# Kernel tuning notes

Measured on AMD Instinct MI355X. Metric: run time of the kernel, lower is better.

## Reference

```python
import jax, jax.numpy as jnp
import numpy as np

N_NODES = 50000
N_EDGES = 800000
F_IN = 32
H = 128
LN_EPS = 1e-5


def _gcn_layer(h, src, tgt, w_self, b_self, w_neigh, b_neigh):
    # h: [N, D]; src/tgt: [E]
    n = h.shape[0]
    self_feat = h @ w_self + b_self                      # [N, Dout]
    src_feat = h[src]                                    # [E, D] gather
    agg = jax.ops.segment_sum(src_feat, tgt, num_segments=n)          # [N, D]
    cnt = jax.ops.segment_sum(jnp.ones((src.shape[0],), h.dtype), tgt,
                              num_segments=n)[:, None]   # [N, 1]
    agg = agg / jnp.maximum(cnt, 1.0)
    return self_feat + agg @ w_neigh + b_neigh


def _layer_norm(x, gamma, beta):
    mu = jnp.mean(x, axis=-1, keepdims=True)
    var = jnp.mean(jnp.square(x - mu), axis=-1, keepdims=True)
    return (x - mu) * jax.lax.rsqrt(var + LN_EPS) * gamma + beta


def setup_inputs() -> dict:
    key = jax.random.key(0)
    ks = jax.random.split(key, 16)
    s_in = 1.0 / np.sqrt(F_IN)
    s_h = 1.0 / np.sqrt(H)
    inp = {
        "x": jax.random.normal(ks[0], (N_NODES, F_IN), jnp.float32),
        "edge_index": jax.random.randint(ks[1], (2, N_EDGES), 0, N_NODES, jnp.int64)
        if jax.config.jax_enable_x64 else
        jax.random.randint(ks[1], (2, N_EDGES), 0, N_NODES, jnp.int32),
        "w_in": jax.random.uniform(ks[2], (F_IN, H), jnp.float32, -s_in, s_in),
        "b_in": jax.random.uniform(ks[3], (H,), jnp.float32, -s_in, s_in),
        "ws0": jax.random.uniform(ks[4], (H, H), jnp.float32, -s_h, s_h),
        "bs0": jax.random.uniform(ks[5], (H,), jnp.float32, -s_h, s_h),
        "wn0": jax.random.uniform(ks[6], (H, H), jnp.float32, -s_h, s_h),
        "bn0": jax.random.uniform(ks[7], (H,), jnp.float32, -s_h, s_h),
        "g0": jnp.ones((H,), jnp.float32),
        "be0": jnp.zeros((H,), jnp.float32),
        "ws1": jax.random.uniform(ks[8], (H, H), jnp.float32, -s_h, s_h),
        "bs1": jax.random.uniform(ks[9], (H,), jnp.float32, -s_h, s_h),
        "wn1": jax.random.uniform(ks[10], (H, H), jnp.float32, -s_h, s_h),
        "bn1": jax.random.uniform(ks[11], (H,), jnp.float32, -s_h, s_h),
        "g1": jnp.ones((H,), jnp.float32),
        "be1": jnp.zeros((H,), jnp.float32),
    }
    return inp


def reference(x, edge_index, w_in, b_in, ws0, bs0, wn0, bn0, g0, be0,
              ws1, bs1, wn1, bn1, g1, be1):
    src, tgt = edge_index[0], edge_index[1]
    h = jax.nn.relu(x @ w_in + b_in)                     # input_proj + relu
    # layer 0 (intermediate): gcn -> LN -> relu -> dropout(eval=id) -> residual
    residual = h
    h = _gcn_layer(h, src, tgt, ws0, bs0, wn0, bn0)
    h = _layer_norm(h, g0, be0)
    h = jax.nn.relu(h) + residual
    # layer 1 (final): gcn -> LN
    h = _gcn_layer(h, src, tgt, ws1, bs1, wn1, bn1)
    h = _layer_norm(h, g1, be1)
    return h
```

## Files before the change

kernel.cpp:

```cpp
#include <hip/hip_runtime.h>

#define H 128
#define CAP 64
typedef unsigned short ushort_t;
typedef __bf16 bf16x8 __attribute__((ext_vector_type(8)));
typedef float f32x4 __attribute__((ext_vector_type(4)));
typedef float f32x2 __attribute__((ext_vector_type(2)));

__device__ __forceinline__ float bf2f(ushort_t b) {
    return __uint_as_float(((unsigned int)b) << 16);
}
__device__ __forceinline__ ushort_t f2bf(float f) {
    unsigned int u = __float_as_uint(f);
    unsigned int r = (u + 0x7fffu + ((u >> 16) & 1u)) >> 16;
    return (ushort_t)r;
}
__device__ __forceinline__ unsigned char f2fp8(float f) {
    int r = __builtin_amdgcn_cvt_pk_fp8_f32(f, f, 0, false);
    return (unsigned char)(r & 0xff);
}

__device__ __forceinline__
void pack_one(int idx, const float* __restrict__ W0, const float* __restrict__ W1,
              const float* __restrict__ b0, const float* __restrict__ b1,
              ushort_t* __restrict__ Wpack, float* __restrict__ bsum,
              int Ksplit, int K)
{
    int total = K * 16;
    if (idx < total) {
        int l = idx & 63, tt = (idx >> 6) & 7, s = idx >> 9;
        int c = tt * 16 + (l & 15);
        int kb = s * 32 + ((l >> 4) & 3) * 8;
#pragma unroll
        for (int j = 0; j < 8; ++j) {
            int k = kb + j;
            float v = (k < Ksplit) ? W0[(size_t)k * H + c]
                                   : W1[(size_t)(k - Ksplit) * H + c];
            Wpack[(size_t)idx * 8 + j] = f2bf(v);
        }
    }
    if (idx < H) bsum[idx] = b0[idx] + (b1 ? b1[idx] : 0.f);
}

__global__ __launch_bounds__(256)
void k_prep(const float* __restrict__ x, ushort_t* __restrict__ xb, int n4,
            const float* __restrict__ w_in, const float* __restrict__ b_in,
            const float* __restrict__ ws0, const float* __restrict__ bs0,
            const float* __restrict__ wn0, const float* __restrict__ bn0,
            const float* __restrict__ ws1, const float* __restrict__ bs1,
            const float* __restrict__ wn1, const float* __restrict__ bn1,
            ushort_t* __restrict__ Wpin, float* __restrict__ bin,
            ushort_t* __restrict__ Wp0, float* __restrict__ bsm0,
            ushort_t* __restrict__ Wp1, float* __restrict__ bsm1,
            int* __restrict__ fl, int N, int gN)
{
    int b = blockIdx.x, t = threadIdx.x;
    if (b < 2) {
        pack_one(b * 256 + t, w_in, w_in, b_in, nullptr, Wpin, bin, 32, 32);
    } else if (b < 18) {
        pack_one((b - 2) * 256 + t, ws0, wn0, bs0, bn0, Wp0, bsm0, 128, 256);
    } else if (b < 34) {
        pack_one((b - 18) * 256 + t, ws1, wn1, bs1, bn1, Wp1, bsm1, 128, 256);
    } else if (b < 34 + gN) {
        int i = (b - 34) * 256 + t;
        if (i < N) fl[i] = 0;
    } else {
        int i = (b - 34 - gN) * 256 + t;
        if (i < n4) {
            float4 v = ((const float4*)x)[i];
            ushort_t* o = xb + (size_t)i * 4;
            o[0] = f2bf(v.x); o[1] = f2bf(v.y); o[2] = f2bf(v.z); o[3] = f2bf(v.w);
        }
    }
}

template<int K, int DO_LN, int RESREL, int RELU, int OUTBF, int HQ>
__global__ __launch_bounds__(256)
void k_gemm_ln(const ushort_t* __restrict__ A, int lda,
               const ushort_t* __restrict__ Wpack,
               const float* __restrict__ bias,
               const float* __restrict__ g, const float* __restrict__ be,
               const ushort_t* __restrict__ resid, int ldr,
               float* __restrict__ Cf, ushort_t* __restrict__ Cb,
               unsigned char* __restrict__ hq,
               int ldc, int M)
{
    constexpr int NS = K / 32;
    __shared__ ushort_t Bs[NS * 8 * 64 * 8];
    const int t = threadIdx.x;
    {
        const uint4* wsrc = (const uint4*)Wpack;
        uint4* wdst = (uint4*)Bs;
        constexpr int CH = K * 16;
#pragma unroll
        for (int i = t; i < CH; i += 256) wdst[i] = wsrc[i];
    }
    __syncthreads();

    const int wave = t >> 6, lane = t & 63;
    const int quad = lane >> 4, l16 = lane & 15;
    const int m0 = blockIdx.x * 128 + wave * 32;

    f32x4 acc[2][8];
#pragma unroll
    for (int mt = 0; mt < 2; ++mt)
#pragma unroll
        for (int nt = 0; nt < 8; ++nt) acc[mt][nt] = (f32x4){0.f, 0.f, 0.f, 0.f};

    bf16x8 afrag[NS][2];
#pragma unroll
    for (int s = 0; s < NS; ++s)
#pragma unroll
        for (int mt = 0; mt < 2; ++mt) {
            int row = m0 + mt * 16 + l16;
            if (row >= M) row = M - 1;
            afrag[s][mt] = *(const bf16x8*)(A + (size_t)row * lda + s * 32 + quad * 8);
        }

    const bf16x8* bfr = (const bf16x8*)Bs;
#pragma unroll
    for (int s = 0; s < NS; ++s)
#pragma unroll
        for (int nt = 0; nt < 8; ++nt) {
            bf16x8 b = bfr[(s * 8 + nt) * 64 + lane];
#pragma unroll
            for (int mt = 0; mt < 2; ++mt)
                acc[mt][nt] = __builtin_amdgcn_mfma_f32_16x16x32_bf16(
                    afrag[s][mt], b, acc[mt][nt], 0, 0, 0);
        }

    float bv[8], gv[8], bev[8];
#pragma unroll
    for (int nt = 0; nt < 8; ++nt) {
        int c = nt * 16 + l16;
        bv[nt] = bias[c];
        if (DO_LN) { gv[nt] = g[c]; bev[nt] = be[c]; }
    }

#pragma unroll
    for (int mt = 0; mt < 2; ++mt)
#pragma unroll
        for (int r = 0; r < 4; ++r) {
            int row = m0 + mt * 16 + quad * 4 + r;
            float v[8];
#pragma unroll
            for (int nt = 0; nt < 8; ++nt) v[nt] = acc[mt][nt][r] + bv[nt];
            if (DO_LN) {
                float s1 = 0.f, s2 = 0.f;
#pragma unroll
                for (int nt = 0; nt < 8; ++nt) { s1 += v[nt]; s2 += v[nt] * v[nt]; }
#pragma unroll
                for (int mk = 1; mk < 16; mk <<= 1) {
                    s1 += __shfl_xor(s1, mk);
                    s2 += __shfl_xor(s2, mk);
                }
                float mu = s1 * (1.f / H);
                float var = s2 * (1.f / H) - mu * mu;
                float rs = rsqrtf(var + 1e-5f);
#pragma unroll
                for (int nt = 0; nt < 8; ++nt)
                    v[nt] = (v[nt] - mu) * rs * gv[nt] + bev[nt];
            }
            if (row < M) {
#pragma unroll
                for (int nt = 0; nt < 8; ++nt) {
                    int c = nt * 16 + l16;
                    float y = v[nt];
                    if (RELU) y = fmaxf(y, 0.f);
                    if (RESREL)
                        y = fmaxf(y, 0.f) + bf2f(resid[(size_t)row * ldr + c]);
                    if (OUTBF) Cb[(size_t)row * ldc + c] = f2bf(y);
                    else       Cf[(size_t)row * ldc + c] = y;
                    if (HQ) hq[(size_t)row * H + c] = f2fp8(y);
                }
            }
        }
}

__global__ __launch_bounds__(256)
void k_agg(const unsigned char* __restrict__ hq, const int* __restrict__ fl,
           const ushort_t* __restrict__ col, ushort_t* __restrict__ out, int n)
{
    int node = blockIdx.x * 4 + (threadIdx.x >> 6);
    if (node >= n) return;
    int lane = threadIdx.x & 63;
    int grp = lane >> 4, li = lane & 15;
    int cnt = fl[node];
    int m = cnt < CAP ? cnt : CAP;
    int beg = node * CAP, end = beg + m;
    float s[8];
#pragma unroll
    for (int j = 0; j < 8; ++j) s[j] = 0.f;

    int e = beg;
    for (; e + 16 <= end; e += 16) {
        uint2 v[4];
#pragma unroll
        for (int q = 0; q < 4; ++q) {
            int r = col[e + 4 * q + grp];
            v[q] = *(const uint2*)(hq + (size_t)r * 128 + li * 8);
        }
#pragma unroll
        for (int q = 0; q < 4; ++q) {
            f32x2 a0 = __builtin_amdgcn_cvt_pk_f32_fp8(v[q].x, false);
            f32x2 a1 = __builtin_amdgcn_cvt_pk_f32_fp8(v[q].x, true);
            f32x2 a2 = __builtin_amdgcn_cvt_pk_f32_fp8(v[q].y, false);
            f32x2 a3 = __builtin_amdgcn_cvt_pk_f32_fp8(v[q].y, true);
            s[0] += a0.x; s[1] += a0.y; s[2] += a1.x; s[3] += a1.y;
            s[4] += a2.x; s[5] += a2.y; s[6] += a3.x; s[7] += a3.y;
        }
    }
    if (e + 8 <= end) {
        uint2 v[2];
#pragma unroll
        for (int q = 0; q < 2; ++q) {
            int r = col[e + 4 * q + grp];
            v[q] = *(const uint2*)(hq + (size_t)r * 128 + li * 8);
        }
#pragma unroll
        for (int q = 0; q < 2; ++q) {
            f32x2 a0 = __builtin_amdgcn_cvt_pk_f32_fp8(v[q].x, false);
            f32x2 a1 = __builtin_amdgcn_cvt_pk_f32_fp8(v[q].x, true);
            f32x2 a2 = __builtin_amdgcn_cvt_pk_f32_fp8(v[q].y, false);
            f32x2 a3 = __builtin_amdgcn_cvt_pk_f32_fp8(v[q].y, true);
            s[0] += a0.x; s[1] += a0.y; s[2] += a1.x; s[3] += a1.y;
            s[4] += a2.x; s[5] += a2.y; s[6] += a3.x; s[7] += a3.y;
        }
        e += 8;
    }
    if (e + 4 <= end) {
        int r = col[e + grp];
        uint2 v0 = *(const uint2*)(hq + (size_t)r * 128 + li * 8);
        f32x2 a0 = __builtin_amdgcn_cvt_pk_f32_fp8(v0.x, false);
        f32x2 a1 = __builtin_amdgcn_cvt_pk_f32_fp8(v0.x, true);
        f32x2 a2 = __builtin_amdgcn_cvt_pk_f32_fp8(v0.y, false);
        f32x2 a3 = __builtin_amdgcn_cvt_pk_f32_fp8(v0.y, true);
        s[0] += a0.x; s[1] += a0.y; s[2] += a1.x; s[3] += a1.y;
        s[4] += a2.x; s[5] += a2.y; s[6] += a3.x; s[7] += a3.y;
        e += 4;
    }
    for (; e < end; ++e) {
        if (grp == 0) {
            int r = col[e];
            uint2 v0 = *(const uint2*)(hq + (size_t)r * 128 + li * 8);
            f32x2 a0 = __builtin_amdgcn_cvt_pk_f32_fp8(v0.x, false);
            f32x2 a1 = __builtin_amdgcn_cvt_pk_f32_fp8(v0.x, true);
            f32x2 a2 = __builtin_amdgcn_cvt_pk_f32_fp8(v0.y, false);
            f32x2 a3 = __builtin_amdgcn_cvt_pk_f32_fp8(v0.y, true);
            s[0] += a0.x; s[1] += a0.y; s[2] += a1.x; s[3] += a1.y;
            s[4] += a2.x; s[5] += a2.y; s[6] += a3.x; s[7] += a3.y;
        }
    }
#pragma unroll
    for (int j = 0; j < 8; ++j) {
        s[j] += __shfl_xor(s[j], 16);
        s[j] += __shfl_xor(s[j], 32);
    }
    if (grp == 0) {
        float inv = 1.f / fmaxf((float)cnt, 1.f);
        uint4 o;
        o.x = ((unsigned)f2bf(s[1] * inv) << 16) | f2bf(s[0] * inv);
        o.y = ((unsigned)f2bf(s[3] * inv) << 16) | f2bf(s[2] * inv);
        o.z = ((unsigned)f2bf(s[5] * inv) << 16) | f2bf(s[4] * inv);
        o.w = ((unsigned)f2bf(s[7] * inv) << 16) | f2bf(s[6] * inv);
        *(uint4*)(out + (size_t)node * 256 + li * 8) = o;
    }
}

#define FILL_CHUNK 4096
__global__ __launch_bounds__(256)
void k_fill(const int* __restrict__ srcs, const int* __restrict__ tgts,
            int* __restrict__ fl, ushort_t* __restrict__ col, int E)
{
    int range = blockIdx.x & 7;
    int chunk = blockIdx.x >> 3;
    int lim = chunk * FILL_CHUNK + FILL_CHUNK;
    if (lim > E) lim = E;
    for (int i = chunk * FILL_CHUNK + threadIdx.x; i < lim; i += 256) {
        int t = tgts[i];
        if ((t >> 13) == range) {
            int p = atomicAdd(&fl[t], 1);
            if (p < CAP) col[t * CAP + p] = (ushort_t)srcs[i];
        }
    }
}

extern "C" void kernel_launch(void* const* d_in, const int* in_sizes, int n_in,
                              void* d_out, int out_size, void* d_ws, size_t ws_size,
                              hipStream_t stream)
{
    const float* x    = (const float*)d_in[0];
    const int*   ei   = (const int*)d_in[1];
    const float* w_in = (const float*)d_in[2];
    const float* b_in = (const float*)d_in[3];
    const float* ws0  = (const float*)d_in[4];
    const float* bs0  = (const float*)d_in[5];
    const float* wn0  = (const float*)d_in[6];
    const float* bn0  = (const float*)d_in[7];
    const float* g0   = (const float*)d_in[8];
    const float* be0  = (const float*)d_in[9];
    const float* ws1  = (const float*)d_in[10];
    const float* bs1  = (const float*)d_in[11];
    const float* wn1  = (const float*)d_in[12];
    const float* bn1  = (const float*)d_in[13];
    const float* g1   = (const float*)d_in[14];
    const float* be1  = (const float*)d_in[15];

    const int N = in_sizes[0] / 32;
    const int E = in_sizes[1] / 2;
    const int* srcs = ei;
    const int* tgts = ei + E;

    char* w = (char*)d_ws;
    ushort_t* Acat0 = (ushort_t*)w;  w += (size_t)N * 256 * 2;
    ushort_t* Acat1 = (ushort_t*)w;  w += (size_t)N * 256 * 2;
    unsigned char* hq0 = (unsigned char*)w;  w += (size_t)N * H;
    unsigned char* hq1 = (unsigned char*)w;  w += (size_t)N * H;
    ushort_t* x_bf  = (ushort_t*)w;  w += (size_t)N * 32 * 2;
    ushort_t* Wpin  = (ushort_t*)w;  w += 32 * H * 2;
    ushort_t* Wp0   = (ushort_t*)w;  w += 256 * H * 2;
    ushort_t* Wp1   = (ushort_t*)w;  w += 256 * H * 2;
    float* bin  = (float*)w;         w += H * 4;
    float* bsm0 = (float*)w;         w += H * 4;
    float* bsm1 = (float*)w;         w += H * 4;
    int* fl     = (int*)w;           w += (size_t)N * 4;
    ushort_t* col = (ushort_t*)w;    w += (size_t)N * CAP * 2;

    int n4 = N * 32 / 4;
    int gN = (N + 255) / 256;
    int gC = (n4 + 255) / 256;
    int gM = (N + 127) / 128;
    int gF = 8 * ((E + FILL_CHUNK - 1) / FILL_CHUNK);

    k_prep<<<34 + gN + gC, 256, 0, stream>>>(
        x, x_bf, n4, w_in, b_in, ws0, bs0, wn0, bn0, ws1, bs1, wn1, bn1,
        Wpin, bin, Wp0, bsm0, Wp1, bsm1, fl, N, gN);

    k_fill<<<gF, 256, 0, stream>>>(srcs, tgts, fl, col, E);

    k_gemm_ln<32, 0, 0, 1, 1, 1><<<gM, 256, 0, stream>>>(
        x_bf, 32, Wpin, bin, nullptr, nullptr, nullptr, 0,
        nullptr, Acat0, hq0, 256, N);

    k_agg<<<(N + 3) / 4, 256, 0, stream>>>(hq0, fl, col, Acat0 + 128, N);
    k_gemm_ln<256, 1, 1, 0, 1, 1><<<gM, 256, 0, stream>>>(
        Acat0, 256, Wp0, bsm0, g0, be0, Acat0, 256,
        nullptr, Acat1, hq1, 256, N);

    k_agg<<<(N + 3) / 4, 256, 0, stream>>>(hq1, fl, col, Acat1 + 128, N);
    k_gemm_ln<256, 1, 0, 0, 0, 0><<<gM, 256, 0, stream>>>(
        Acat1, 256, Wp1, bsm1, g1, be1, nullptr, 0,
        (float*)d_out, nullptr, nullptr, H, N);
}
```

Baseline: 227.9 us.

## Fuse neighbor aggregation into per-layer GEMM+LayerNorm kernel

Merges the separate gather-mean aggregation kernel and the GEMM+LN kernel into one per-layer kernel. Each wave aggregates its 16 nodes into shared memory and then feeds them straight into the MFMA as the second half of K. This removes the bf16 agg round trip through global memory and two launches. In exchange each wave serialises over 16 nodes of gather work, uses 64-row blocks, and stages the weights into LDS in two halves with extra barriers, which may reduce latency hiding for the gathers.

```diff
diff --git a/kernel.cpp b/kernel.cpp
--- a/kernel.cpp
+++ b/kernel.cpp
@@ -2,6 +2,7 @@
 
 #define H 128
 #define CAP 64
+#define FILL_CHUNK 4096
 typedef unsigned short ushort_t;
 typedef __bf16 bf16x8 __attribute__((ext_vector_type(8)));
 typedef float f32x4 __attribute__((ext_vector_type(4)));
@@ -74,200 +75,6 @@
     }
 }
 
-template<int K, int DO_LN, int RESREL, int RELU, int OUTBF, int HQ>
-__global__ __launch_bounds__(256)
-void k_gemm_ln(const ushort_t* __restrict__ A, int lda,
-               const ushort_t* __restrict__ Wpack,
-               const float* __restrict__ bias,
-               const float* __restrict__ g, const float* __restrict__ be,
-               const ushort_t* __restrict__ resid, int ldr,
-               float* __restrict__ Cf, ushort_t* __restrict__ Cb,
-               unsigned char* __restrict__ hq,
-               int ldc, int M)
-{
-    constexpr int NS = K / 32;
-    __shared__ ushort_t Bs[NS * 8 * 64 * 8];
-    const int t = threadIdx.x;
-    {
-        const uint4* wsrc = (const uint4*)Wpack;
-        uint4* wdst = (uint4*)Bs;
-        constexpr int CH = K * 16;
-#pragma unroll
-        for (int i = t; i < CH; i += 256) wdst[i] = wsrc[i];
-    }
-    __syncthreads();
-
-    const int wave = t >> 6, lane = t & 63;
-    const int quad = lane >> 4, l16 = lane & 15;
-    const int m0 = blockIdx.x * 128 + wave * 32;
-
-    f32x4 acc[2][8];
-#pragma unroll
-    for (int mt = 0; mt < 2; ++mt)
-#pragma unroll
-        for (int nt = 0; nt < 8; ++nt) acc[mt][nt] = (f32x4){0.f, 0.f, 0.f, 0.f};
-
-    bf16x8 afrag[NS][2];
-#pragma unroll
-    for (int s = 0; s < NS; ++s)
-#pragma unroll
-        for (int mt = 0; mt < 2; ++mt) {
-            int row = m0 + mt * 16 + l16;
-            if (row >= M) row = M - 1;
-            afrag[s][mt] = *(const bf16x8*)(A + (size_t)row * lda + s * 32 + quad * 8);
-        }
-
-    const bf16x8* bfr = (const bf16x8*)Bs;
-#pragma unroll
-    for (int s = 0; s < NS; ++s)
-#pragma unroll
-        for (int nt = 0; nt < 8; ++nt) {
-            bf16x8 b = bfr[(s * 8 + nt) * 64 + lane];
-#pragma unroll
-            for (int mt = 0; mt < 2; ++mt)
-                acc[mt][nt] = __builtin_amdgcn_mfma_f32_16x16x32_bf16(
-                    afrag[s][mt], b, acc[mt][nt], 0, 0, 0);
-        }
-
-    float bv[8], gv[8], bev[8];
-#pragma unroll
-    for (int nt = 0; nt < 8; ++nt) {
-        int c = nt * 16 + l16;
-        bv[nt] = bias[c];
-        if (DO_LN) { gv[nt] = g[c]; bev[nt] = be[c]; }
-    }
-
-#pragma unroll
-    for (int mt = 0; mt < 2; ++mt)
-#pragma unroll
-        for (int r = 0; r < 4; ++r) {
-            int row = m0 + mt * 16 + quad * 4 + r;
-            float v[8];
-#pragma unroll
-            for (int nt = 0; nt < 8; ++nt) v[nt] = acc[mt][nt][r] + bv[nt];
-            if (DO_LN) {
-                float s1 = 0.f, s2 = 0.f;
-#pragma unroll
-                for (int nt = 0; nt < 8; ++nt) { s1 += v[nt]; s2 += v[nt] * v[nt]; }
-#pragma unroll
-                for (int mk = 1; mk < 16; mk <<= 1) {
-                    s1 += __shfl_xor(s1, mk);
-                    s2 += __shfl_xor(s2, mk);
-                }
-                float mu = s1 * (1.f / H);
-                float var = s2 * (1.f / H) - mu * mu;
-                float rs = rsqrtf(var + 1e-5f);
-#pragma unroll
-                for (int nt = 0; nt < 8; ++nt)
-                    v[nt] = (v[nt] - mu) * rs * gv[nt] + bev[nt];
-            }
-            if (row < M) {
-#pragma unroll
-                for (int nt = 0; nt < 8; ++nt) {
-                    int c = nt * 16 + l16;
-                    float y = v[nt];
-                    if (RELU) y = fmaxf(y, 0.f);
-                    if (RESREL)
-                        y = fmaxf(y, 0.f) + bf2f(resid[(size_t)row * ldr + c]);
-                    if (OUTBF) Cb[(size_t)row * ldc + c] = f2bf(y);
-                    else       Cf[(size_t)row * ldc + c] = y;
-                    if (HQ) hq[(size_t)row * H + c] = f2fp8(y);
-                }
-            }
-        }
-}
-
-__global__ __launch_bounds__(256)
-void k_agg(const unsigned char* __restrict__ hq, const int* __restrict__ fl,
-           const ushort_t* __restrict__ col, ushort_t* __restrict__ out, int n)
-{
-    int node = blockIdx.x * 4 + (threadIdx.x >> 6);
-    if (node >= n) return;
-    int lane = threadIdx.x & 63;
-    int grp = lane >> 4, li = lane & 15;
-    int cnt = fl[node];
-    int m = cnt < CAP ? cnt : CAP;
-    int beg = node * CAP, end = beg + m;
-    float s[8];
-#pragma unroll
-    for (int j = 0; j < 8; ++j) s[j] = 0.f;
-
-    int e = beg;
-    for (; e + 16 <= end; e += 16) {
-        uint2 v[4];
-#pragma unroll
-        for (int q = 0; q < 4; ++q) {
-            int r = col[e + 4 * q + grp];
-            v[q] = *(const uint2*)(hq + (size_t)r * 128 + li * 8);
-        }
-#pragma unroll
-        for (int q = 0; q < 4; ++q) {
-            f32x2 a0 = __builtin_amdgcn_cvt_pk_f32_fp8(v[q].x, false);
-            f32x2 a1 = __builtin_amdgcn_cvt_pk_f32_fp8(v[q].x, true);
-            f32x2 a2 = __builtin_amdgcn_cvt_pk_f32_fp8(v[q].y, false);
-            f32x2 a3 = __builtin_amdgcn_cvt_pk_f32_fp8(v[q].y, true);
-            s[0] += a0.x; s[1] += a0.y; s[2] += a1.x; s[3] += a1.y;
-            s[4] += a2.x; s[5] += a2.y; s[6] += a3.x; s[7] += a3.y;
-        }
-    }
-    if (e + 8 <= end) {
-        uint2 v[2];
-#pragma unroll
-        for (int q = 0; q < 2; ++q) {
-            int r = col[e + 4 * q + grp];
-            v[q] = *(const uint2*)(hq + (size_t)r * 128 + li * 8);
-        }
-#pragma unroll
-        for (int q = 0; q < 2; ++q) {
-            f32x2 a0 = __builtin_amdgcn_cvt_pk_f32_fp8(v[q].x, false);
-            f32x2 a1 = __builtin_amdgcn_cvt_pk_f32_fp8(v[q].x, true);
-            f32x2 a2 = __builtin_amdgcn_cvt_pk_f32_fp8(v[q].y, false);
-            f32x2 a3 = __builtin_amdgcn_cvt_pk_f32_fp8(v[q].y, true);
-            s[0] += a0.x; s[1] += a0.y; s[2] += a1.x; s[3] += a1.y;
-            s[4] += a2.x; s[5] += a2.y; s[6] += a3.x; s[7] += a3.y;
-        }
-        e += 8;
-    }
-    if (e + 4 <= end) {
-        int r = col[e + grp];
-        uint2 v0 = *(const uint2*)(hq + (size_t)r * 128 + li * 8);
-        f32x2 a0 = __builtin_amdgcn_cvt_pk_f32_fp8(v0.x, false);
-        f32x2 a1 = __builtin_amdgcn_cvt_pk_f32_fp8(v0.x, true);
-        f32x2 a2 = __builtin_amdgcn_cvt_pk_f32_fp8(v0.y, false);
-        f32x2 a3 = __builtin_amdgcn_cvt_pk_f32_fp8(v0.y, true);
-        s[0] += a0.x; s[1] += a0.y; s[2] += a1.x; s[3] += a1.y;
-        s[4] += a2.x; s[5] += a2.y; s[6] += a3.x; s[7] += a3.y;
-        e += 4;
-    }
-    for (; e < end; ++e) {
-        if (grp == 0) {
-            int r = col[e];
-            uint2 v0 = *(const uint2*)(hq + (size_t)r * 128 + li * 8);
-            f32x2 a0 = __builtin_amdgcn_cvt_pk_f32_fp8(v0.x, false);
-            f32x2 a1 = __builtin_amdgcn_cvt_pk_f32_fp8(v0.x, true);
-            f32x2 a2 = __builtin_amdgcn_cvt_pk_f32_fp8(v0.y, false);
-            f32x2 a3 = __builtin_amdgcn_cvt_pk_f32_fp8(v0.y, true);
-            s[0] += a0.x; s[1] += a0.y; s[2] += a1.x; s[3] += a1.y;
-            s[4] += a2.x; s[5] += a2.y; s[6] += a3.x; s[7] += a3.y;
-        }
-    }
-#pragma unroll
-    for (int j = 0; j < 8; ++j) {
-        s[j] += __shfl_xor(s[j], 16);
-        s[j] += __shfl_xor(s[j], 32);
-    }
-    if (grp == 0) {
-        float inv = 1.f / fmaxf((float)cnt, 1.f);
-        uint4 o;
-        o.x = ((unsigned)f2bf(s[1] * inv) << 16) | f2bf(s[0] * inv);
-        o.y = ((unsigned)f2bf(s[3] * inv) << 16) | f2bf(s[2] * inv);
-        o.z = ((unsigned)f2bf(s[5] * inv) << 16) | f2bf(s[4] * inv);
-        o.w = ((unsigned)f2bf(s[7] * inv) << 16) | f2bf(s[6] * inv);
-        *(uint4*)(out + (size_t)node * 256 + li * 8) = o;
-    }
-}
-
-#define FILL_CHUNK 4096
 __global__ __launch_bounds__(256)
 void k_fill(const int* __restrict__ srcs, const int* __restrict__ tgts,
             int* __restrict__ fl, ushort_t* __restrict__ col, int E)
@@ -281,6 +88,253 @@
         if ((t >> 13) == range) {
             int p = atomicAdd(&fl[t], 1);
             if (p < CAP) col[t * CAP + p] = (ushort_t)srcs[i];
+        }
+    }
+}
+
+__global__ __launch_bounds__(256)
+void k_gin(const ushort_t* __restrict__ A,
+           const ushort_t* __restrict__ Wpack, const float* __restrict__ bias,
+           ushort_t* __restrict__ hout, unsigned char* __restrict__ hqout, int M)
+{
+    __shared__ ushort_t Bs[512 * 8];
+    const int t = threadIdx.x;
+    {
+        const uint4* wsrc = (const uint4*)Wpack;
+        uint4* wdst = (uint4*)Bs;
+#pragma unroll
+        for (int i = t; i < 512; i += 256) wdst[i] = wsrc[i];
+    }
+    __syncthreads();
+
+    const int wave = t >> 6, lane = t & 63;
+    const int quad = lane >> 4, l16 = lane & 15;
+    const int m0 = blockIdx.x * 128 + wave * 32;
+    const bf16x8* bfr = (const bf16x8*)Bs;
+
+    f32x4 acc[2][8];
+#pragma unroll
+    for (int mt = 0; mt < 2; ++mt)
+#pragma unroll
+        for (int nt = 0; nt < 8; ++nt) acc[mt][nt] = (f32x4){0.f, 0.f, 0.f, 0.f};
+
+    bf16x8 afrag[2];
+#pragma unroll
+    for (int mt = 0; mt < 2; ++mt) {
+        int row = m0 + mt * 16 + l16;
+        if (row >= M) row = M - 1;
+        afrag[mt] = *(const bf16x8*)(A + (size_t)row * 32 + quad * 8);
+    }
+#pragma unroll
+    for (int nt = 0; nt < 8; ++nt) {
+        bf16x8 b = bfr[nt * 64 + lane];
+#pragma unroll
+        for (int mt = 0; mt < 2; ++mt)
+            acc[mt][nt] = __builtin_amdgcn_mfma_f32_16x16x32_bf16(
+                afrag[mt], b, acc[mt][nt], 0, 0, 0);
+    }
+
+    float bv[8];
+#pragma unroll
+    for (int nt = 0; nt < 8; ++nt) bv[nt] = bias[nt * 16 + l16];
+
+#pragma unroll
+    for (int mt = 0; mt < 2; ++mt)
+#pragma unroll
+        for (int r = 0; r < 4; ++r) {
+            int row = m0 + mt * 16 + quad * 4 + r;
+            if (row < M) {
+#pragma unroll
+                for (int nt = 0; nt < 8; ++nt) {
+                    int c = nt * 16 + l16;
+                    float y = fmaxf(acc[mt][nt][r] + bv[nt], 0.f);
+                    hout[(size_t)row * H + c] = f2bf(y);
+                    hqout[(size_t)row * H + c] = f2fp8(y);
+                }
+            }
+        }
+}
+
+template<int L0>
+__global__ __launch_bounds__(256)
+void k_layer(const ushort_t* __restrict__ h, const unsigned char* __restrict__ hq,
+             const int* __restrict__ fl, const ushort_t* __restrict__ col,
+             const ushort_t* __restrict__ Wpack, const float* __restrict__ bias,
+             const float* __restrict__ g, const float* __restrict__ be,
+             ushort_t* __restrict__ hout, unsigned char* __restrict__ hqout,
+             float* __restrict__ fout, int M)
+{
+    __shared__ ushort_t Bs[4 * 512 * 8];
+    __shared__ ushort_t aggBuf[4][16 * 136];
+    const int t = threadIdx.x, wave = t >> 6, lane = t & 63;
+    const int quad = lane >> 4, l16 = lane & 15;
+    const int m0 = blockIdx.x * 64 + wave * 16;
+
+    bf16x8 afrag[8];
+#pragma unroll
+    for (int s = 0; s < 4; ++s) {
+        int row = m0 + l16; if (row >= M) row = M - 1;
+        afrag[s] = *(const bf16x8*)(h + (size_t)row * H + s * 32 + quad * 8);
+    }
+
+    {
+        const uint4* wsrc = (const uint4*)Wpack;
+        uint4* wdst = (uint4*)Bs;
+#pragma unroll
+        for (int i = t; i < 2048; i += 256) wdst[i] = wsrc[i];
+    }
+
+    ushort_t* ab = aggBuf[wave];
+    for (int j = 0; j < 16; ++j) {
+        int node = m0 + j;
+        if (node >= M) break;
+        int cnt = fl[node];
+        int m = cnt < CAP ? cnt : CAP;
+        int beg = node * CAP;
+        float s[8];
+#pragma unroll
+        for (int k = 0; k < 8; ++k) s[k] = 0.f;
+        int e = 0;
+        for (; e + 16 <= m; e += 16) {
+            uint2 v[4];
+#pragma unroll
+            for (int q = 0; q < 4; ++q) {
+                int r = col[beg + e + 4 * q + quad];
+                v[q] = *(const uint2*)(hq + (size_t)r * H + l16 * 8);
+            }
+#pragma unroll
+            for (int q = 0; q < 4; ++q) {
+                f32x2 a0 = __builtin_amdgcn_cvt_pk_f32_fp8(v[q].x, false);
+                f32x2 a1 = __builtin_amdgcn_cvt_pk_f32_fp8(v[q].x, true);
+                f32x2 a2 = __builtin_amdgcn_cvt_pk_f32_fp8(v[q].y, false);
+                f32x2 a3 = __builtin_amdgcn_cvt_pk_f32_fp8(v[q].y, true);
+                s[0] += a0.x; s[1] += a0.y; s[2] += a1.x; s[3] += a1.y;
+                s[4] += a2.x; s[5] += a2.y; s[6] += a3.x; s[7] += a3.y;
+            }
+        }
+        if (e + 8 <= m) {
+            uint2 v[2];
+#pragma unroll
+            for (int q = 0; q < 2; ++q) {
+                int r = col[beg + e + 4 * q + quad];
+                v[q] = *(const uint2*)(hq + (size_t)r * H + l16 * 8);
+            }
+#pragma unroll
+            for (int q = 0; q < 2; ++q) {
+                f32x2 a0 = __builtin_amdgcn_cvt_pk_f32_fp8(v[q].x, false);
+                f32x2 a1 = __builtin_amdgcn_cvt_pk_f32_fp8(v[q].x, true);
+                f32x2 a2 = __builtin_amdgcn_cvt_pk_f32_fp8(v[q].y, false);
+                f32x2 a3 = __builtin_amdgcn_cvt_pk_f32_fp8(v[q].y, true);
+                s[0] += a0.x; s[1] += a0.y; s[2] += a1.x; s[3] += a1.y;
+                s[4] += a2.x; s[5] += a2.y; s[6] += a3.x; s[7] += a3.y;
+            }
+            e += 8;
+        }
+        if (e + 4 <= m) {
+            int r = col[beg + e + quad];
+            uint2 v0 = *(const uint2*)(hq + (size_t)r * H + l16 * 8);
+            f32x2 a0 = __builtin_amdgcn_cvt_pk_f32_fp8(v0.x, false);
+            f32x2 a1 = __builtin_amdgcn_cvt_pk_f32_fp8(v0.x, true);
+            f32x2 a2 = __builtin_amdgcn_cvt_pk_f32_fp8(v0.y, false);
+            f32x2 a3 = __builtin_amdgcn_cvt_pk_f32_fp8(v0.y, true);
+            s[0] += a0.x; s[1] += a0.y; s[2] += a1.x; s[3] += a1.y;
+            s[4] += a2.x; s[5] += a2.y; s[6] += a3.x; s[7] += a3.y;
+            e += 4;
+        }
+        if (quad < m - e) {
+            int r = col[beg + e + quad];
+            uint2 v0 = *(const uint2*)(hq + (size_t)r * H + l16 * 8);
+            f32x2 a0 = __builtin_amdgcn_cvt_pk_f32_fp8(v0.x, false);
+            f32x2 a1 = __builtin_amdgcn_cvt_pk_f32_fp8(v0.x, true);
+            f32x2 a2 = __builtin_amdgcn_cvt_pk_f32_fp8(v0.y, false);
+            f32x2 a3 = __builtin_amdgcn_cvt_pk_f32_fp8(v0.y, true);
+            s[0] += a0.x; s[1] += a0.y; s[2] += a1.x; s[3] += a1.y;
+            s[4] += a2.x; s[5] += a2.y; s[6] += a3.x; s[7] += a3.y;
+        }
+#pragma unroll
+        for (int k = 0; k < 8; ++k) {
+            s[k] += __shfl_xor(s[k], 16);
+            s[k] += __shfl_xor(s[k], 32);
+        }
+        if (quad == 0) {
+            float inv = 1.f / fmaxf((float)cnt, 1.f);
+            uint4 o;
+            o.x = ((unsigned)f2bf(s[1] * inv) << 16) | f2bf(s[0] * inv);
+            o.y = ((unsigned)f2bf(s[3] * inv) << 16) | f2bf(s[2] * inv);
+            o.z = ((unsigned)f2bf(s[5] * inv) << 16) | f2bf(s[4] * inv);
+            o.w = ((unsigned)f2bf(s[7] * inv) << 16) | f2bf(s[6] * inv);
+            *(uint4*)(ab + j * 136 + l16 * 8) = o;
+        }
+    }
+
+#pragma unroll
+    for (int s = 4; s < 8; ++s)
+        afrag[s] = *(const bf16x8*)(ab + l16 * 136 + (s - 4) * 32 + quad * 8);
+
+    f32x4 acc[8];
+#pragma unroll
+    for (int nt = 0; nt < 8; ++nt) acc[nt] = (f32x4){0.f, 0.f, 0.f, 0.f};
+
+    const bf16x8* bfr = (const bf16x8*)Bs;
+    __syncthreads();
+#pragma unroll
+    for (int s = 0; s < 4; ++s)
+#pragma unroll
+        for (int nt = 0; nt < 8; ++nt)
+            acc[nt] = __builtin_amdgcn_mfma_f32_16x16x32_bf16(
+                afrag[s], bfr[(s * 8 + nt) * 64 + lane], acc[nt], 0, 0, 0);
+    __syncthreads();
+    {
+        const uint4* wsrc = (const uint4*)Wpack + 2048;
+        uint4* wdst = (uint4*)Bs;
+#pragma unroll
+        for (int i = t; i < 2048; i += 256) wdst[i] = wsrc[i];
+    }
+    __syncthreads();
+#pragma unroll
+    for (int s = 4; s < 8; ++s)
+#pragma unroll
+        for (int nt = 0; nt < 8; ++nt)
+            acc[nt] = __builtin_amdgcn_mfma_f32_16x16x32_bf16(
+                afrag[s], bfr[((s - 4) * 8 + nt) * 64 + lane], acc[nt], 0, 0, 0);
+
+    float bv[8], gv[8], bev[8];
+#pragma unroll
+    for (int nt = 0; nt < 8; ++nt) {
+        int c = nt * 16 + l16;
+        bv[nt] = bias[c];
+        gv[nt] = g[c]; bev[nt] = be[c];
+    }
+#pragma unroll
+    for (int r = 0; r < 4; ++r) {
+        int row = m0 + quad * 4 + r;
+        float v[8];
+#pragma unroll
+        for (int nt = 0; nt < 8; ++nt) v[nt] = acc[nt][r] + bv[nt];
+        float s1 = 0.f, s2 = 0.f;
+#pragma unroll
+        for (int nt = 0; nt < 8; ++nt) { s1 += v[nt]; s2 += v[nt] * v[nt]; }
+#pragma unroll
+        for (int mk = 1; mk < 16; mk <<= 1) {
+            s1 += __shfl_xor(s1, mk);
+            s2 += __shfl_xor(s2, mk);
+        }
+        float mu = s1 * (1.f / H);
+        float var = s2 * (1.f / H) - mu * mu;
+        float rs = rsqrtf(var + 1e-5f);
+        if (row < M) {
+#pragma unroll
+            for (int nt = 0; nt < 8; ++nt) {
+                int c = nt * 16 + l16;
+                float y = (v[nt] - mu) * rs * gv[nt] + bev[nt];
+                if (L0) {
+                    y = fmaxf(y, 0.f) + bf2f(h[(size_t)row * H + c]);
+                    hout[(size_t)row * H + c] = f2bf(y);
+                    hqout[(size_t)row * H + c] = f2fp8(y);
+                } else {
+                    fout[(size_t)row * H + c] = y;
+                }
+            }
         }
     }
 }
@@ -312,24 +366,25 @@
     const int* tgts = ei + E;
 
     char* w = (char*)d_ws;
-    ushort_t* Acat0 = (ushort_t*)w;  w += (size_t)N * 256 * 2;
-    ushort_t* Acat1 = (ushort_t*)w;  w += (size_t)N * 256 * 2;
-    unsigned char* hq0 = (unsigned char*)w;  w += (size_t)N * H;
-    unsigned char* hq1 = (unsigned char*)w;  w += (size_t)N * H;
-    ushort_t* x_bf  = (ushort_t*)w;  w += (size_t)N * 32 * 2;
-    ushort_t* Wpin  = (ushort_t*)w;  w += 32 * H * 2;
-    ushort_t* Wp0   = (ushort_t*)w;  w += 256 * H * 2;
-    ushort_t* Wp1   = (ushort_t*)w;  w += 256 * H * 2;
-    float* bin  = (float*)w;         w += H * 4;
-    float* bsm0 = (float*)w;         w += H * 4;
-    float* bsm1 = (float*)w;         w += H * 4;
-    int* fl     = (int*)w;           w += (size_t)N * 4;
-    ushort_t* col = (ushort_t*)w;    w += (size_t)N * CAP * 2;
+    ushort_t* h0   = (ushort_t*)w;          w += (size_t)N * H * 2;
+    ushort_t* h1   = (ushort_t*)w;          w += (size_t)N * H * 2;
+    unsigned char* hq0 = (unsigned char*)w; w += (size_t)N * H;
+    unsigned char* hq1 = (unsigned char*)w; w += (size_t)N * H;
+    ushort_t* x_bf = (ushort_t*)w;          w += (size_t)N * 32 * 2;
+    ushort_t* Wpin = (ushort_t*)w;          w += 32 * H * 2;
+    ushort_t* Wp0  = (ushort_t*)w;          w += 256 * H * 2;
+    ushort_t* Wp1  = (ushort_t*)w;          w += 256 * H * 2;
+    float* bin  = (float*)w;                w += H * 4;
+    float* bsm0 = (float*)w;                w += H * 4;
+    float* bsm1 = (float*)w;                w += H * 4;
+    int* fl     = (int*)w;                  w += (size_t)N * 4;
+    ushort_t* col = (ushort_t*)w;           w += (size_t)N * CAP * 2;
 
     int n4 = N * 32 / 4;
     int gN = (N + 255) / 256;
     int gC = (n4 + 255) / 256;
     int gM = (N + 127) / 128;
+    int gL = (N + 63) / 64;
     int gF = 8 * ((E + FILL_CHUNK - 1) / FILL_CHUNK);
 
     k_prep<<<34 + gN + gC, 256, 0, stream>>>(
@@ -338,17 +393,11 @@
 
     k_fill<<<gF, 256, 0, stream>>>(srcs, tgts, fl, col, E);
 
-    k_gemm_ln<32, 0, 0, 1, 1, 1><<<gM, 256, 0, stream>>>(
-        x_bf, 32, Wpin, bin, nullptr, nullptr, nullptr, 0,
-        nullptr, Acat0, hq0, 256, N);
-
-    k_agg<<<(N + 3) / 4, 256, 0, stream>>>(hq0, fl, col, Acat0 + 128, N);
-    k_gemm_ln<256, 1, 1, 0, 1, 1><<<gM, 256, 0, stream>>>(
-        Acat0, 256, Wp0, bsm0, g0, be0, Acat0, 256,
-        nullptr, Acat1, hq1, 256, N);
-
-    k_agg<<<(N + 3) / 4, 256, 0, stream>>>(hq1, fl, col, Acat1 + 128, N);
-    k_gemm_ln<256, 1, 0, 0, 0, 0><<<gM, 256, 0, stream>>>(
-        Acat1, 256, Wp1, bsm1, g1, be1, nullptr, 0,
-        (float*)d_out, nullptr, nullptr, H, N);
-}
+    k_gin<<<gM, 256, 0, stream>>>(x_bf, Wpin, bin, h0, hq0, N);
+
+    k_layer<1><<<gL, 256, 0, stream>>>(h0, hq0, fl, col, Wp0, bsm0, g0, be0,
+                                       h1, hq1, nullptr, N);
+
+    k_layer<0><<<gL, 256, 0, stream>>>(h1, hq1, fl, col, Wp1, bsm1, g1, be1,
+                                       nullptr, nullptr, (float*)d_out, N);
+}
```

Result: slower. 302.4 us (+32.7%).
